# Kernel optimization log

Hardware: AMD Instinct MI355X
Metric: run time of the kernel (lower is better)

Reference implementation:

```python
import jax, jax.numpy as jnp
import numpy as np

N = 40000   # nodes
E = 640000  # edges (before self-loops)
D = 128     # hidden_dim (in = out per head)
H = 2       # heads
C = 128     # per-head out channels
L = 2       # num_layers
NEG_SLOPE = 0.2


def setup_inputs() -> dict:
    key = jax.random.key(0)
    k0, k1, k2, k3, k4 = jax.random.split(key, 5)
    scale = 1.0 / np.sqrt(D).astype(np.float32)
    x = jax.random.normal(k0, (N, D), jnp.float32)
    edge_index = jax.random.randint(k1, (2, E), 0, N, jnp.int32)
    W = jax.random.normal(k2, (L, H * C, D), jnp.float32) * scale
    att_src = jax.random.normal(k3, (L, H, C), jnp.float32) * scale
    att_dst = jax.random.normal(k4, (L, H, C), jnp.float32) * scale
    bias = jnp.zeros((L, D), jnp.float32)
    return {"x": x, "edge_index": edge_index, "W": W,
            "att_src": att_src, "att_dst": att_dst, "bias": bias}


def _gat_layer(x, src, dst, W, a_s, a_d, b):
    # Linear projection -> per-head features [N, H, C]
    h = (x @ W.T).reshape(N, H, C)
    # Per-node attention logits [N, H]
    e_src = (h * a_s).sum(-1)
    e_dst = (h * a_d).sum(-1)
    # Per-edge logits: edge (src j -> dst i)
    e = jax.nn.leaky_relu(e_src[src] + e_dst[dst], NEG_SLOPE)  # [Etot, H]
    # Segment softmax over incoming edges of each dst node (stable)
    m = jax.lax.stop_gradient(jax.ops.segment_max(e, dst, num_segments=N))
    p = jnp.exp(e - m[dst])
    s = jax.ops.segment_sum(p, dst, num_segments=N)
    alpha = p / s[dst]                                          # [Etot, H]
    # Weighted scatter-add aggregation [N, H, C]
    out = jax.ops.segment_sum(h[src] * alpha[:, :, None], dst, num_segments=N)
    # concat=False -> mean over heads, then bias
    return out.mean(axis=1) + b


def reference(x, edge_index, W, att_src, att_dst, bias):
    loops = jnp.arange(N, dtype=edge_index.dtype)
    src = jnp.concatenate([edge_index[0], loops])  # add self-loops (PyG default)
    dst = jnp.concatenate([edge_index[1], loops])
    xs = [x]
    h = x
    for l in range(L):
        h = jax.nn.elu(_gat_layer(h, src, dst, W[l], att_src[l], att_dst[l], bias[l]))
        xs.append(h)  # eval mode: dropout is identity
    return tuple(xs)
```

## Files before the change

kernel.cpp:

```cpp
#include <hip/hip_runtime.h>
#include <hip/hip_bf16.h>
#include <hip/hip_fp8.h>

#define N_NODES 40000
#define N_EDGES 640000
#define ETOT    (N_NODES + N_EDGES)
#define D_DIM   128
#define HC      256
#define NEG     0.2f
#define CAP     64

typedef short short8v __attribute__((ext_vector_type(8)));
typedef float f32x4 __attribute__((ext_vector_type(4)));
typedef float f32x2 __attribute__((ext_vector_type(2)));

static __device__ __forceinline__ float bf2f(unsigned short u) {
    return __uint_as_float(((unsigned)u) << 16);
}
static __device__ __forceinline__ unsigned short f2bf(float f) {
    __hip_bfloat16 b = __float2bfloat16(f);
    unsigned short r;
    __builtin_memcpy(&r, &b, 2);
    return r;
}
static __device__ __forceinline__ unsigned char f2fp8(float f) {
    __hip_fp8_e4m3 v(f);
    return (unsigned char)v.__x;
}
static __device__ __forceinline__ unsigned int pk4fp8(float a, float b, float c, float d) {
#if __has_builtin(__builtin_amdgcn_cvt_pk_fp8_f32)
    int w = __builtin_amdgcn_cvt_pk_fp8_f32(a, b, 0, false);
    w = __builtin_amdgcn_cvt_pk_fp8_f32(c, d, w, true);
    return (unsigned int)w;
#else
    return (unsigned int)f2fp8(a) | ((unsigned int)f2fp8(b) << 8) |
           ((unsigned int)f2fp8(c) << 16) | ((unsigned int)f2fp8(d) << 24);
#endif
}
static __device__ __forceinline__ void cvt4fp8(unsigned int w, float* f) {
#if __has_builtin(__builtin_amdgcn_cvt_pk_f32_fp8)
    f32x2 lo = __builtin_amdgcn_cvt_pk_f32_fp8(w, false);
    f32x2 hi = __builtin_amdgcn_cvt_pk_f32_fp8(w, true);
    f[0] = lo[0]; f[1] = lo[1]; f[2] = hi[0]; f[3] = hi[1];
#else
    for (int i = 0; i < 4; i++) {
        __hip_fp8_e4m3 v; v.__x = (unsigned char)(w >> (8 * i));
        f[i] = (float)v;
    }
#endif
}

#define SCT_BLKS 665
#define WCV_BLKS 64
#define CPY_BLKS 5000
__global__ __launch_bounds__(256) void prep_k(const int* __restrict__ ei, int* __restrict__ deg,
                                              unsigned short* __restrict__ csrc,
                                              const float4* __restrict__ W, ushort4* __restrict__ wb,
                                              const float4* __restrict__ x, float4* __restrict__ out,
                                              ushort4* __restrict__ xb) {
    const int b = blockIdx.x;
    if (b < SCT_BLKS) {
        const int e0 = b * 1024 + threadIdx.x;
#pragma unroll
        for (int u = 0; u < 4; u++) {
            const int e = e0 + u * 256;
            if (e < ETOT) {
                int ss, dd;
                if (e < N_EDGES) { ss = ei[e]; dd = ei[N_EDGES + e]; }
                else             { ss = e - N_EDGES; dd = ss; }
                int pos = atomicAdd(&deg[dd], 1);
                if (pos < CAP) csrc[dd * CAP + pos] = (unsigned short)ss;
            }
        }
    } else if (b < SCT_BLKS + WCV_BLKS) {
        int i = (b - SCT_BLKS) * 256 + threadIdx.x;
        float4 v = W[i];
        ushort4 u; u.x = f2bf(v.x); u.y = f2bf(v.y); u.z = f2bf(v.z); u.w = f2bf(v.w);
        wb[i] = u;
    } else {
        int i = (b - SCT_BLKS - WCV_BLKS) * 256 + threadIdx.x;
        float4 v = x[i];
        out[i] = v;
        ushort4 u; u.x = f2bf(v.x); u.y = f2bf(v.y); u.z = f2bf(v.z); u.w = f2bf(v.w);
        xb[i] = u;
    }
}

__global__ __launch_bounds__(256) void gemm_enode_k(const unsigned short* __restrict__ A,
                                                    const unsigned short* __restrict__ Wb,
                                                    unsigned char* __restrict__ h8,
                                                    const float* __restrict__ a_s,
                                                    const float* __restrict__ a_d,
                                                    float4* __restrict__ esd) {
    __shared__ unsigned short wsd[HC * D_DIM];
    const int t = threadIdx.x;
    const int wv = t >> 6;
    const int lane = t & 63;
    const int bm = blockIdx.x * 64 + wv * 16;
    const int l16 = lane & 15;
    const int kg = lane >> 4;
#pragma unroll
    for (int i = 0; i < 16; i++) {
        const int idx = i * 256 + t;
        const int r = idx >> 4, c = idx & 15;
        short8v v = *(const short8v*)(Wb + (size_t)idx * 8);
        *(short8v*)(wsd + r * 128 + ((c ^ (r & 15)) * 8)) = v;
    }
    __syncthreads();
    f32x4 acc[16] = {};
#pragma unroll
    for (int kk = 0; kk < 4; kk++) {
        const int k0 = kk * 32 + kg * 8;
        short8v af = *(const short8v*)(A + (size_t)(bm + l16) * 128 + k0);
        const int cc = kk * 4 + kg;
#pragma unroll
        for (int n = 0; n < 16; n++) {
            const int r = n * 16 + l16;
            short8v bf_ = *(const short8v*)(wsd + r * 128 + (((cc ^ l16) & 15) * 8));
            acc[n] = __builtin_amdgcn_mfma_f32_16x16x32_bf16(af, bf_, acc[n], 0, 0, 0);
        }
    }
    float asv[16], adv[16];
#pragma unroll
    for (int n = 0; n < 16; n++) {
        asv[n] = a_s[n * 16 + l16];
        adv[n] = a_d[n * 16 + l16];
    }
#pragma unroll
    for (int r = 0; r < 4; r++) {
        const int orow = bm + kg * 4 + r;
        float es0 = 0.f, es1 = 0.f, ed0 = 0.f, ed1 = 0.f;
        unsigned int pk[4];
#pragma unroll
        for (int nq = 0; nq < 4; nq++)
            pk[nq] = pk4fp8(acc[nq * 4][r], acc[nq * 4 + 1][r],
                            acc[nq * 4 + 2][r], acc[nq * 4 + 3][r]);
#pragma unroll
        for (int n = 0; n < 8; n++)  { es0 += acc[n][r] * asv[n]; ed0 += acc[n][r] * adv[n]; }
#pragma unroll
        for (int n = 8; n < 16; n++) { es1 += acc[n][r] * asv[n]; ed1 += acc[n][r] * adv[n]; }
        *(uint4*)(h8 + (size_t)orow * 256 + l16 * 16) = make_uint4(pk[0], pk[1], pk[2], pk[3]);
#pragma unroll
        for (int m = 1; m < 16; m <<= 1) {
            es0 += __shfl_xor(es0, m, 16);
            es1 += __shfl_xor(es1, m, 16);
            ed0 += __shfl_xor(ed0, m, 16);
            ed1 += __shfl_xor(ed1, m, 16);
        }
        if (l16 == 0) esd[orow] = make_float4(es0, es1, ed0, ed1);
    }
}

template <int WX>
__global__ __launch_bounds__(256) void agg_k(const unsigned char* __restrict__ h8,
                                             const float4* __restrict__ esd,
                                             const int* __restrict__ deg,
                                             const unsigned short* __restrict__ csrc,
                                             const float* __restrict__ bias, float* __restrict__ out,
                                             unsigned short* __restrict__ xbf) {
    __shared__ unsigned short sS[4][64];
    __shared__ float sP[4][2][64];
    const int lane = threadIdx.x & 63;
    const int wid = threadIdx.x >> 6;
    const int d = blockIdx.x * 4 + wid;
    if (d >= N_NODES) return;
    const int dg = min(deg[d], CAP);
    const int rbase = d * CAP;
    const int q = lane >> 4;
    const int l16 = lane & 15;
    const float4 edv = esd[d];
    float acc[16] = {};
    float sp0 = 0.f, sp1 = 0.f;
    for (int c0 = 0; c0 < dg; c0 += 64) {
        const int cnt = min(64, dg - c0);
        const int padded = (cnt + 15) & ~15;
        if (lane < padded) {
            unsigned short s = 0;
            float p0 = 0.f, p1 = 0.f;
            if (lane < cnt) {
                s = csrc[rbase + c0 + lane];
                const float4 e4 = esd[s];
                float e0 = e4.x + edv.z; e0 = e0 > 0.f ? e0 : NEG * e0;
                float e1 = e4.y + edv.w; e1 = e1 > 0.f ? e1 : NEG * e1;
                p0 = __expf(fminf(e0, 60.f));
                p1 = __expf(fminf(e1, 60.f));
                sp0 += p0; sp1 += p1;
            }
            sS[wid][lane] = s;
            sP[wid][0][lane] = p0;
            sP[wid][1][lane] = p1;
        }
        asm volatile("s_waitcnt lgkmcnt(0)" ::: "memory");
        const int iters = padded >> 2;
        for (int i0 = 0; i0 < iters; i0 += 4) {
            float pj0[4], pj1[4];
            uint4 hv[4];
#pragma unroll
            for (int u = 0; u < 4; u++) {
                const int j = 4 * (i0 + u) + q;
                const int sj = sS[wid][j];
                pj0[u] = sP[wid][0][j];
                pj1[u] = sP[wid][1][j];
                hv[u] = *(const uint4*)(h8 + (size_t)sj * 256 + l16 * 16);
            }
#pragma unroll
            for (int u = 0; u < 4; u++) {
                float f[16];
                cvt4fp8(hv[u].x, f);
                cvt4fp8(hv[u].y, f + 4);
                cvt4fp8(hv[u].z, f + 8);
                cvt4fp8(hv[u].w, f + 12);
#pragma unroll
                for (int k = 0; k < 16; k++)
                    acc[k] += (k < 8 ? pj0[u] : pj1[u]) * f[k];
            }
        }
    }
#pragma unroll
    for (int k = 0; k < 16; k++) {
        acc[k] += __shfl_xor(acc[k], 16, 64);
        acc[k] += __shfl_xor(acc[k], 32, 64);
    }
#pragma unroll
    for (int m = 1; m < 64; m <<= 1) {
        sp0 += __shfl_xor(sp0, m, 64);
        sp1 += __shfl_xor(sp1, m, 64);
    }
    const float inv0 = 1.f / sp0;
    const float inv1 = 1.f / sp1;
    float res[8];
#pragma unroll
    for (int k = 0; k < 8; k++)
        res[k] = (acc[k] * inv0 + acc[k + 8] * inv1) * 0.5f;
    if (lane < 16) {
#pragma unroll
        for (int k = 0; k < 8; k++) {
            const int ch = k * 16 + l16;
            float v = res[k] + bias[ch];
            v = v > 0.f ? v : (__expf(v) - 1.f);
            out[(size_t)d * D_DIM + ch] = v;
            if (WX) xbf[(size_t)d * D_DIM + ch] = f2bf(v);
        }
    }
}

extern "C" void kernel_launch(void* const* d_in, const int* in_sizes, int n_in,
                              void* d_out, int out_size, void* d_ws, size_t ws_size,
                              hipStream_t stream) {
    const float* x  = (const float*)d_in[0];
    const int* ei   = (const int*)d_in[1];
    const float* W  = (const float*)d_in[2];
    const float* as_ = (const float*)d_in[3];
    const float* ad_ = (const float*)d_in[4];
    const float* bias = (const float*)d_in[5];
    float* out = (float*)d_out;

    char* ws = (char*)d_ws;
    size_t off = 0;
    auto alloc = [&](size_t bytes) -> void* {
        void* p = ws + off;
        off = (off + bytes + 255) & ~(size_t)255;
        return p;
    };
    unsigned char* h8 = (unsigned char*)alloc((size_t)N_NODES * HC);
    unsigned short* xbf = (unsigned short*)alloc((size_t)N_NODES * D_DIM * 2);
    float* esd = (float*)alloc((size_t)N_NODES * 16);
    unsigned short* wbf = (unsigned short*)alloc((size_t)2 * HC * D_DIM * 2);
    int* deg  = (int*)alloc((size_t)N_NODES * 4);
    unsigned short* csrc = (unsigned short*)alloc((size_t)N_NODES * CAP * 2);

    hipMemsetAsync(deg, 0, (size_t)N_NODES * 4, stream);
    prep_k<<<SCT_BLKS + WCV_BLKS + CPY_BLKS, 256, 0, stream>>>(
        ei, deg, csrc, (const float4*)W, (ushort4*)wbf, (const float4*)x, (float4*)out, (ushort4*)xbf);

    const size_t nd = (size_t)N_NODES * D_DIM;
    const int AGG_BLKS = (N_NODES + 3) / 4;
    for (int l = 0; l < 2; l++) {
        float* ol = out + (size_t)(l + 1) * nd;
        gemm_enode_k<<<625, 256, 0, stream>>>(xbf, wbf + (size_t)l * HC * D_DIM,
                                              h8, as_ + l * HC, ad_ + l * HC, (float4*)esd);
        if (l == 0)
            agg_k<1><<<AGG_BLKS, 256, 0, stream>>>(h8, (const float4*)esd, deg, csrc,
                                                   bias, ol, xbf);
        else
            agg_k<0><<<AGG_BLKS, 256, 0, stream>>>(h8, (const float4*)esd, deg, csrc,
                                                   bias + D_DIM, ol, xbf);
    }
}
```

Baseline: 160.1 us.

## Split edge bucketing into sharded count, prefix merge, and fill passes

Replaces the single atomic scatter pass with three steps. The first counts degrees into 8 sharded counter arrays, chosen by block index, to spread atomic contention. A merge kernel then turns the shards into per-shard offsets and a total degree. A fill pass scatters source ids using atomics on the sharded offsets. This is meant to cut contention on hot degree counters, but it reads the edge list twice and adds two kernel launches and a larger memset.

```diff
diff --git a/kernel.cpp b/kernel.cpp
--- a/kernel.cpp
+++ b/kernel.cpp
@@ -9,6 +9,7 @@
 #define HC      256
 #define NEG     0.2f
 #define CAP     64
+#define NB1     157
 
 typedef short short8v __attribute__((ext_vector_type(8)));
 typedef float f32x4 __attribute__((ext_vector_type(4)));
@@ -50,39 +51,67 @@
 #endif
 }
 
-#define SCT_BLKS 665
+#define CNT_BLKS 665
 #define WCV_BLKS 64
 #define CPY_BLKS 5000
-__global__ __launch_bounds__(256) void prep_k(const int* __restrict__ ei, int* __restrict__ deg,
-                                              unsigned short* __restrict__ csrc,
+__global__ __launch_bounds__(256) void prep_k(const int* __restrict__ ei, int* __restrict__ deg8,
                                               const float4* __restrict__ W, ushort4* __restrict__ wb,
                                               const float4* __restrict__ x, float4* __restrict__ out,
                                               ushort4* __restrict__ xb) {
     const int b = blockIdx.x;
-    if (b < SCT_BLKS) {
+    if (b < CNT_BLKS) {
+        int* dg = deg8 + (size_t)(b & 7) * N_NODES;
         const int e0 = b * 1024 + threadIdx.x;
 #pragma unroll
         for (int u = 0; u < 4; u++) {
             const int e = e0 + u * 256;
             if (e < ETOT) {
-                int ss, dd;
-                if (e < N_EDGES) { ss = ei[e]; dd = ei[N_EDGES + e]; }
-                else             { ss = e - N_EDGES; dd = ss; }
-                int pos = atomicAdd(&deg[dd], 1);
-                if (pos < CAP) csrc[dd * CAP + pos] = (unsigned short)ss;
+                int dd = (e < N_EDGES) ? ei[N_EDGES + e] : (e - N_EDGES);
+                atomicAdd(&dg[dd], 1);
             }
         }
-    } else if (b < SCT_BLKS + WCV_BLKS) {
-        int i = (b - SCT_BLKS) * 256 + threadIdx.x;
+    } else if (b < CNT_BLKS + WCV_BLKS) {
+        int i = (b - CNT_BLKS) * 256 + threadIdx.x;
         float4 v = W[i];
         ushort4 u; u.x = f2bf(v.x); u.y = f2bf(v.y); u.z = f2bf(v.z); u.w = f2bf(v.w);
         wb[i] = u;
     } else {
-        int i = (b - SCT_BLKS - WCV_BLKS) * 256 + threadIdx.x;
+        int i = (b - CNT_BLKS - WCV_BLKS) * 256 + threadIdx.x;
         float4 v = x[i];
         out[i] = v;
         ushort4 u; u.x = f2bf(v.x); u.y = f2bf(v.y); u.z = f2bf(v.z); u.w = f2bf(v.w);
         xb[i] = u;
+    }
+}
+
+__global__ __launch_bounds__(256) void merge_k(int* __restrict__ deg8, int* __restrict__ deg) {
+    const int d = blockIdx.x * 256 + threadIdx.x;
+    if (d >= N_NODES) return;
+    int tot = 0;
+#pragma unroll
+    for (int j = 0; j < 8; j++) {
+        const int c = deg8[(size_t)j * N_NODES + d];
+        deg8[(size_t)j * N_NODES + d] = tot;
+        tot += c;
+    }
+    deg[d] = tot;
+}
+
+__global__ __launch_bounds__(256) void fill_k(const int* __restrict__ ei, int* __restrict__ deg8,
+                                              unsigned short* __restrict__ csrc) {
+    const int b = blockIdx.x;
+    int* dg = deg8 + (size_t)(b & 7) * N_NODES;
+    const int e0 = b * 1024 + threadIdx.x;
+#pragma unroll
+    for (int u = 0; u < 4; u++) {
+        const int e = e0 + u * 256;
+        if (e < ETOT) {
+            int ss, dd;
+            if (e < N_EDGES) { ss = ei[e]; dd = ei[N_EDGES + e]; }
+            else             { ss = e - N_EDGES; dd = ss; }
+            int pos = atomicAdd(&dg[dd], 1);
+            if (pos < CAP) csrc[dd * CAP + pos] = (unsigned short)ss;
+        }
     }
 }
 
@@ -266,12 +295,15 @@
     unsigned short* xbf = (unsigned short*)alloc((size_t)N_NODES * D_DIM * 2);
     float* esd = (float*)alloc((size_t)N_NODES * 16);
     unsigned short* wbf = (unsigned short*)alloc((size_t)2 * HC * D_DIM * 2);
+    int* deg8 = (int*)alloc((size_t)8 * N_NODES * 4);
     int* deg  = (int*)alloc((size_t)N_NODES * 4);
     unsigned short* csrc = (unsigned short*)alloc((size_t)N_NODES * CAP * 2);
 
-    hipMemsetAsync(deg, 0, (size_t)N_NODES * 4, stream);
-    prep_k<<<SCT_BLKS + WCV_BLKS + CPY_BLKS, 256, 0, stream>>>(
-        ei, deg, csrc, (const float4*)W, (ushort4*)wbf, (const float4*)x, (float4*)out, (ushort4*)xbf);
+    hipMemsetAsync(deg8, 0, (size_t)8 * N_NODES * 4, stream);
+    prep_k<<<CNT_BLKS + WCV_BLKS + CPY_BLKS, 256, 0, stream>>>(
+        ei, deg8, (const float4*)W, (ushort4*)wbf, (const float4*)x, (float4*)out, (ushort4*)xbf);
+    merge_k<<<NB1, 256, 0, stream>>>(deg8, deg);
+    fill_k<<<CNT_BLKS, 256, 0, stream>>>(ei, deg8, csrc);
 
     const size_t nd = (size_t)N_NODES * D_DIM;
     const int AGG_BLKS = (N_NODES + 3) / 4;
```

Result: slower. 192.3 us (+20.1%).

## Fuse layer-0 projection GEMM into the prep kernel alongside CSR scatter

Applied to the files above, without the earlier changes.

The layer-0 GEMM plus attention-logit computation moves into the prep kernel as a separate range of blocks. It reads fp32 x and W directly and converts them to bf16 on the fly, so one kernel launch disappears and the GEMM can overlap with the edge scatter atomics. Only layer-1 weights are still converted to bf16, and the copy blocks now handle two float4 per thread. In exchange, every block of the fused kernel reserves the 64KB shared-memory tile, which limits how many scatter and copy blocks can be resident on a CU at once.

```diff
diff --git a/kernel.cpp b/kernel.cpp
--- a/kernel.cpp
+++ b/kernel.cpp
@@ -51,16 +51,25 @@
 }
 
 #define SCT_BLKS 665
-#define WCV_BLKS 64
-#define CPY_BLKS 5000
-__global__ __launch_bounds__(256) void prep_k(const int* __restrict__ ei, int* __restrict__ deg,
-                                              unsigned short* __restrict__ csrc,
-                                              const float4* __restrict__ W, ushort4* __restrict__ wb,
-                                              const float4* __restrict__ x, float4* __restrict__ out,
-                                              ushort4* __restrict__ xb) {
+#define G0_BLKS  625
+#define WCV_BLKS 32
+#define CPY_BLKS 2500
+__global__ __launch_bounds__(256) void fused0_k(const int* __restrict__ ei, int* __restrict__ deg,
+                                                unsigned short* __restrict__ csrc,
+                                                const float* __restrict__ x,
+                                                const float* __restrict__ W,
+                                                unsigned char* __restrict__ h8,
+                                                const float* __restrict__ a_s,
+                                                const float* __restrict__ a_d,
+                                                float4* __restrict__ esd,
+                                                unsigned short* __restrict__ wbf,
+                                                float4* __restrict__ out,
+                                                ushort4* __restrict__ xb) {
+    __shared__ unsigned short wsd[HC * D_DIM];
     const int b = blockIdx.x;
+    const int t = threadIdx.x;
     if (b < SCT_BLKS) {
-        const int e0 = b * 1024 + threadIdx.x;
+        const int e0 = b * 1024 + t;
 #pragma unroll
         for (int u = 0; u < 4; u++) {
             const int e = e0 + u * 256;
@@ -72,17 +81,93 @@
                 if (pos < CAP) csrc[dd * CAP + pos] = (unsigned short)ss;
             }
         }
-    } else if (b < SCT_BLKS + WCV_BLKS) {
-        int i = (b - SCT_BLKS) * 256 + threadIdx.x;
-        float4 v = W[i];
+    } else if (b < SCT_BLKS + G0_BLKS) {
+        const int blk = b - SCT_BLKS;
+        const int wv = t >> 6;
+        const int lane = t & 63;
+        const int bm = blk * 64 + wv * 16;
+        const int l16 = lane & 15;
+        const int kg = lane >> 4;
+#pragma unroll
+        for (int i = 0; i < 16; i++) {
+            const int idx = i * 256 + t;
+            const int r = idx >> 4, c = idx & 15;
+            const float* wp = W + (size_t)idx * 8;
+            float4 w0 = *(const float4*)wp;
+            float4 w1 = *(const float4*)(wp + 4);
+            short8v v;
+            v[0] = (short)f2bf(w0.x); v[1] = (short)f2bf(w0.y);
+            v[2] = (short)f2bf(w0.z); v[3] = (short)f2bf(w0.w);
+            v[4] = (short)f2bf(w1.x); v[5] = (short)f2bf(w1.y);
+            v[6] = (short)f2bf(w1.z); v[7] = (short)f2bf(w1.w);
+            *(short8v*)(wsd + r * 128 + ((c ^ (r & 15)) * 8)) = v;
+        }
+        __syncthreads();
+        f32x4 acc[16] = {};
+#pragma unroll
+        for (int kk = 0; kk < 4; kk++) {
+            const int k0 = kk * 32 + kg * 8;
+            const float* ap = x + (size_t)(bm + l16) * 128 + k0;
+            float4 a0 = *(const float4*)ap;
+            float4 a1 = *(const float4*)(ap + 4);
+            short8v af;
+            af[0] = (short)f2bf(a0.x); af[1] = (short)f2bf(a0.y);
+            af[2] = (short)f2bf(a0.z); af[3] = (short)f2bf(a0.w);
+            af[4] = (short)f2bf(a1.x); af[5] = (short)f2bf(a1.y);
+            af[6] = (short)f2bf(a1.z); af[7] = (short)f2bf(a1.w);
+            const int cc = kk * 4 + kg;
+#pragma unroll
+            for (int n = 0; n < 16; n++) {
+                const int r = n * 16 + l16;
+                short8v bf_ = *(const short8v*)(wsd + r * 128 + (((cc ^ l16) & 15) * 8));
+                acc[n] = __builtin_amdgcn_mfma_f32_16x16x32_bf16(af, bf_, acc[n], 0, 0, 0);
+            }
+        }
+        float asv[16], adv[16];
+#pragma unroll
+        for (int n = 0; n < 16; n++) {
+            asv[n] = a_s[n * 16 + l16];
+            adv[n] = a_d[n * 16 + l16];
+        }
+#pragma unroll
+        for (int r = 0; r < 4; r++) {
+            const int orow = bm + kg * 4 + r;
+            float es0 = 0.f, es1 = 0.f, ed0 = 0.f, ed1 = 0.f;
+            unsigned int pk[4];
+#pragma unroll
+            for (int nq = 0; nq < 4; nq++)
+                pk[nq] = pk4fp8(acc[nq * 4][r], acc[nq * 4 + 1][r],
+                                acc[nq * 4 + 2][r], acc[nq * 4 + 3][r]);
+#pragma unroll
+            for (int n = 0; n < 8; n++)  { es0 += acc[n][r] * asv[n]; ed0 += acc[n][r] * adv[n]; }
+#pragma unroll
+            for (int n = 8; n < 16; n++) { es1 += acc[n][r] * asv[n]; ed1 += acc[n][r] * adv[n]; }
+            *(uint4*)(h8 + (size_t)orow * 256 + l16 * 16) = make_uint4(pk[0], pk[1], pk[2], pk[3]);
+#pragma unroll
+            for (int m = 1; m < 16; m <<= 1) {
+                es0 += __shfl_xor(es0, m, 16);
+                es1 += __shfl_xor(es1, m, 16);
+                ed0 += __shfl_xor(ed0, m, 16);
+                ed1 += __shfl_xor(ed1, m, 16);
+            }
+            if (l16 == 0) esd[orow] = make_float4(es0, es1, ed0, ed1);
+        }
+    } else if (b < SCT_BLKS + G0_BLKS + WCV_BLKS) {
+        const int i = (b - SCT_BLKS - G0_BLKS) * 256 + t;
+        float4 v = ((const float4*)W)[8192 + i];
         ushort4 u; u.x = f2bf(v.x); u.y = f2bf(v.y); u.z = f2bf(v.z); u.w = f2bf(v.w);
-        wb[i] = u;
+        ((ushort4*)wbf)[i] = u;
     } else {
-        int i = (b - SCT_BLKS - WCV_BLKS) * 256 + threadIdx.x;
-        float4 v = x[i];
-        out[i] = v;
-        ushort4 u; u.x = f2bf(v.x); u.y = f2bf(v.y); u.z = f2bf(v.z); u.w = f2bf(v.w);
-        xb[i] = u;
+        const float4* x4 = (const float4*)x;
+        const int i0 = ((b - SCT_BLKS - G0_BLKS - WCV_BLKS) * 256 + t) * 2;
+#pragma unroll
+        for (int u = 0; u < 2; u++) {
+            const int i = i0 + u;
+            float4 v = x4[i];
+            out[i] = v;
+            ushort4 uu; uu.x = f2bf(v.x); uu.y = f2bf(v.y); uu.z = f2bf(v.z); uu.w = f2bf(v.w);
+            xb[i] = uu;
+        }
     }
 }
 
@@ -265,25 +350,19 @@
     unsigned char* h8 = (unsigned char*)alloc((size_t)N_NODES * HC);
     unsigned short* xbf = (unsigned short*)alloc((size_t)N_NODES * D_DIM * 2);
     float* esd = (float*)alloc((size_t)N_NODES * 16);
-    unsigned short* wbf = (unsigned short*)alloc((size_t)2 * HC * D_DIM * 2);
+    unsigned short* wbf = (unsigned short*)alloc((size_t)HC * D_DIM * 2);
     int* deg  = (int*)alloc((size_t)N_NODES * 4);
     unsigned short* csrc = (unsigned short*)alloc((size_t)N_NODES * CAP * 2);
 
     hipMemsetAsync(deg, 0, (size_t)N_NODES * 4, stream);
-    prep_k<<<SCT_BLKS + WCV_BLKS + CPY_BLKS, 256, 0, stream>>>(
-        ei, deg, csrc, (const float4*)W, (ushort4*)wbf, (const float4*)x, (float4*)out, (ushort4*)xbf);
+    fused0_k<<<SCT_BLKS + G0_BLKS + WCV_BLKS + CPY_BLKS, 256, 0, stream>>>(
+        ei, deg, csrc, x, W, h8, as_, ad_, (float4*)esd, wbf, (float4*)out, (ushort4*)xbf);
 
     const size_t nd = (size_t)N_NODES * D_DIM;
     const int AGG_BLKS = (N_NODES + 3) / 4;
-    for (int l = 0; l < 2; l++) {
-        float* ol = out + (size_t)(l + 1) * nd;
-        gemm_enode_k<<<625, 256, 0, stream>>>(xbf, wbf + (size_t)l * HC * D_DIM,
-                                              h8, as_ + l * HC, ad_ + l * HC, (float4*)esd);
-        if (l == 0)
-            agg_k<1><<<AGG_BLKS, 256, 0, stream>>>(h8, (const float4*)esd, deg, csrc,
-                                                   bias, ol, xbf);
-        else
-            agg_k<0><<<AGG_BLKS, 256, 0, stream>>>(h8, (const float4*)esd, deg, csrc,
-                                                   bias + D_DIM, ol, xbf);
-    }
-}
+    agg_k<1><<<AGG_BLKS, 256, 0, stream>>>(h8, (const float4*)esd, deg, csrc,
+                                           bias, out + nd, xbf);
+    gemm_enode_k<<<625, 256, 0, stream>>>(xbf, wbf, h8, as_ + HC, ad_ + HC, (float4*)esd);
+    agg_k<0><<<AGG_BLKS, 256, 0, stream>>>(h8, (const float4*)esd, deg, csrc,
+                                           bias + D_DIM, out + 2 * nd, xbf);
+}
```

Measured after the change: 153.8 us. 1.04x faster.
